# Performance work log

Measured on AMD Instinct MI355X. Metric: run time of the kernel, lower is better.

## Reference

```python
import jax, jax.numpy as jnp
import numpy as np

T = 4096          # total tokens across ragged segments
H = 4096          # hidden_size
I = 11008         # intermediate_size
R = 16            # lora_rank
A = 4             # number of adapters (segments)


def setup_inputs() -> dict:
    key = jax.random.key(0)
    ks = jax.random.split(key, 12)
    inp = {
        "x": jax.random.normal(ks[0], (T, H), jnp.float32),
        "gate_w": jax.random.normal(ks[1], (I, H), jnp.float32) * (1.0 / np.sqrt(H)),
        "up_w": jax.random.normal(ks[2], (I, H), jnp.float32) * (1.0 / np.sqrt(H)),
        "down_w": jax.random.normal(ks[3], (H, I), jnp.float32) * (1.0 / np.sqrt(I)),
        "gate_wa": jax.random.normal(ks[4], (A, H, R), jnp.float32) * 0.01,
        "gate_wb": jax.random.normal(ks[5], (A, R, I), jnp.float32) * 0.01,
        "up_wa": jax.random.normal(ks[6], (A, H, R), jnp.float32) * 0.01,
        "up_wb": jax.random.normal(ks[7], (A, R, I), jnp.float32) * 0.01,
        "down_wa": jax.random.normal(ks[8], (A, I, R), jnp.float32) * 0.01,
        "down_wb": jax.random.normal(ks[9], (A, R, H), jnp.float32) * 0.01,
        "seg_ids": jnp.sort(jax.random.randint(ks[10], (T,), 0, A, jnp.int32)),
    }
    return inp


def _add_lora(y, inp, wa, wb, mask):
    # Segment-batched low-rank GEMM (Punica/S-LoRA add_lora):
    # for token t in segment a:  y[t] += inp[t] @ wa[a] @ wb[a]
    # mask: [T, A] one-hot of token->adapter assignment.
    # [A, T, R]: project into rank space for every adapter (R tiny), mask out
    xa = jnp.einsum('th,ahr->tar', inp, wa) * mask[:, :, None]   # [T, A, R]
    a, r = wb.shape[0], wb.shape[1]
    # collapse (A, R) so the expansion is one GEMM, no [A, T, out] intermediate
    delta = xa.reshape(inp.shape[0], a * r) @ wb.reshape(a * r, wb.shape[2])
    return y + delta


def reference(x, gate_w, up_w, down_w, gate_wa, gate_wb, up_wa, up_wb,
              down_wa, down_wb, seg_ids):
    mask = (seg_ids[:, None] == jnp.arange(A, dtype=seg_ids.dtype)[None, :]
            ).astype(x.dtype)                                    # [T, A]
    gate = x @ gate_w.T                                          # [T, I]
    gate = _add_lora(gate, x, gate_wa, gate_wb, mask)
    gate = jax.nn.silu(gate)
    up = x @ up_w.T                                              # [T, I]
    up = _add_lora(up, x, up_wa, up_wb, mask)
    t = gate * up
    down = t @ down_w.T                                          # [T, H]
    down = _add_lora(down, t, down_wa, down_wb, mask)
    return down
```

## Files before the change

kernel.cpp:

```cpp
#include <hip/hip_runtime.h>

#define T_TOK 4096
#define HID   4096
#define IMD   11008

using f32x4  = __attribute__((ext_vector_type(4))) float;
using bf16x8 = __attribute__((ext_vector_type(8))) __bf16;
union FragCast { int4 i; bf16x8 b; };

__device__ __forceinline__ unsigned f2bf_bits(float f) {
  unsigned u = __float_as_uint(f);
  return (u + 0x7fffu + ((u >> 16) & 1u)) >> 16;
}
__device__ __forceinline__ float bf2f(short s) {
  return __uint_as_float(((unsigned)(unsigned short)s) << 16);
}
__device__ __forceinline__ int4 cvt8(const float4 f0, const float4 f1) {
  int4 r;
  r.x = f2bf_bits(f0.x) | (f2bf_bits(f0.y) << 16);
  r.y = f2bf_bits(f0.z) | (f2bf_bits(f0.w) << 16);
  r.z = f2bf_bits(f1.x) | (f2bf_bits(f1.y) << 16);
  r.w = f2bf_bits(f1.z) | (f2bf_bits(f1.w) << 16);
  return r;
}
__device__ __forceinline__ void gload16(const void* g, void* l) {
  __builtin_amdgcn_global_load_lds(
      (__attribute__((address_space(1))) void*)g,
      (__attribute__((address_space(3))) void*)l, 16, 0, 0);
}

__global__ void cvt_pad(const float* __restrict__ in, short* __restrict__ out,
                        int C8, int CT, long ldin, long ldout) {
  long r = blockIdx.x;
  const float4* s = (const float4*)(in + r * ldin);
  int4* d = (int4*)(out + r * ldout);
  for (int c = threadIdx.x; c < CT; c += blockDim.x)
    d[c] = (c < C8) ? cvt8(s[2 * c], s[2 * c + 1]) : int4{0, 0, 0, 0};
}

__global__ void build_wbT_pad(const float* __restrict__ wb,
                              short* __restrict__ out, int N, long ldout,
                              long K) {
  int n = blockIdx.x * blockDim.x + threadIdx.x;
  int ar = blockIdx.y;
  if (n < N) out[(long)n * ldout + K + ar] = (short)f2bf_bits(wb[(long)ar * N + n]);
}

template <int KD, int NOUT>
__global__ __launch_bounds__(256)
void lora_proj(const short* __restrict__ Abf, long ldA,
               const float* __restrict__ wa0, const float* __restrict__ wa1,
               const int* __restrict__ seg, short* out0, long ld0, short* out1,
               long ld1) {
  __shared__ __align__(16) short rowbuf[KD];
  __shared__ float part[NOUT][4][16];
  int t = blockIdx.x, tid = threadIdx.x;
  int a = seg[t];
  const int4* src = (const int4*)(Abf + (long)t * ldA);
  for (int c = tid; c < KD / 8; c += 256) ((int4*)rowbuf)[c] = src[c];
  __syncthreads();
  int w = tid >> 6, l = tid & 63;
  int r = l & 15, g = l >> 4;
  const int HW = KD / 4;
  float s0 = 0.f, s1 = 0.f;
  const float* p0 = wa0 + (long)a * KD * 16 + r;
  const float* p1 = (NOUT == 2) ? (wa1 + (long)a * KD * 16 + r) : nullptr;
  int h = w * HW + g;
  for (int k = 0; k < HW / 4; ++k, h += 4) {
    float xv = bf2f(rowbuf[h]);
    s0 = fmaf(xv, p0[(long)h * 16], s0);
    if (NOUT == 2) s1 = fmaf(xv, p1[(long)h * 16], s1);
  }
  s0 += __shfl_xor(s0, 16); s0 += __shfl_xor(s0, 32);
  if (NOUT == 2) { s1 += __shfl_xor(s1, 16); s1 += __shfl_xor(s1, 32); }
  if (l < 16) { part[0][w][r] = s0; if (NOUT == 2) part[1][w][r] = s1; }
  __syncthreads();
  if (tid < 64 * NOUT) {
    int m = tid >> 6, ar = tid & 63;
    float v = 0.f;
    if ((ar >> 4) == a) {
      int r2 = ar & 15;
      v = part[m][0][r2] + part[m][1][r2] + part[m][2][r2] + part[m][3][r2];
    }
    short b = (short)f2bf_bits(v);
    if (m == 0) out0[(long)t * ld0 + ar] = b;
    else        out1[(long)t * ld1 + ar] = b;
  }
}

template <int MODE>
__global__ __launch_bounds__(512, 2)
void gemm_gu(const short* __restrict__ A, const short* __restrict__ B,
             const short* __restrict__ gbuf, short* __restrict__ outB,
             int tilesPerXcd, long ldK, int iters, long ldo) {
  extern __shared__ __align__(16) char smem[];

  int xcd = blockIdx.x & 7, loc = blockIdx.x >> 3;
  int tid = threadIdx.x;
  int l = tid & 63, wid = tid >> 6;
  int wr = wid >> 2, wc = wid & 3;
  int lrow = l & 15, lhi = l >> 4, md = lrow & 7;
  const int rr0 = tid >> 3;
  const long cOff = (long)(((tid & 7) ^ (rr0 & 7)) * 8);

  const int csel0 = (lhi ^ md) * 16;
  const int csel1 = ((4 + lhi) ^ md) * 16;

  const short* pA; const short* pB; long row0, col0;
  auto setTile = [&](int idxInXcd) {
    int gt = xcd * tilesPerXcd + idxInXcd;
    row0 = (long)(gt & 15) * 256;
    col0 = (long)(gt >> 4) * 256;
    pA = A + (row0 + rr0) * ldK + cOff;
    pB = B + (col0 + rr0) * ldK + cOff;
  };
  auto stA = [&](int bi, int h, int kt) {
    char* d = smem + bi * 32768 + tid * 16;
    const short* s = pA + (long)kt * 64 + (long)(2 * h) * 64 * ldK;
    gload16(s, d + (2 * h) * 8192);
    gload16(s + (long)64 * ldK, d + (2 * h + 1) * 8192);
  };
  auto stB = [&](int bi, int h, int kt) {
    char* d = smem + 98304 + bi * 32768 + tid * 16;
    const short* s = pB + (long)kt * 64 + (long)(2 * h) * 64 * ldK;
    gload16(s, d + (2 * h) * 8192);
    gload16(s + (long)64 * ldK, d + (2 * h + 1) * 8192);
  };
  auto prologue = [&]() {
    stA(0, 0, 0); stA(0, 1, 0);
    stB(0, 0, 0); stB(0, 1, 0);
    stA(1, 0, 1); stA(1, 1, 1);
  };

  f32x4 zr = {0.f, 0.f, 0.f, 0.f};

  int r = loc;
  setTile(r);
  prologue();

  while (true) {
    f32x4 acc[8][4];
#pragma unroll
    for (int mi = 0; mi < 8; ++mi)
#pragma unroll
      for (int ni = 0; ni < 4; ++ni) acc[mi][ni] = zr;

    asm volatile("s_waitcnt vmcnt(4)" ::: "memory");
    asm volatile("s_barrier" ::: "memory");

    int ca = 0;
#pragma unroll 1
    for (int t = 0; t < iters; ++t) {
      const char* Ab = smem + ca * 32768;
      const char* Bb = smem + 98304 + (t & 1) * 32768;
      int na2 = (ca >= 1) ? ca - 1 : 2;
      int nb1 = (t + 1) & 1;
      bf16x8 bF[4][2];

#pragma unroll
      for (int p = 0; p < 4; ++p) {
        if (p == 0) {
#pragma unroll
          for (int ni = 0; ni < 4; ++ni) {
            const char* base = Bb + (wc * 64 + ni * 16 + lrow) * 128;
            FragCast f0, f1;
            f0.i = *(const int4*)(base + csel0);
            f1.i = *(const int4*)(base + csel1);
            bF[ni][0] = f0.b; bF[ni][1] = f1.b;
          }
        }
        bf16x8 aF[2][2];
#pragma unroll
        for (int m2 = 0; m2 < 2; ++m2) {
          const char* base = Ab + (wr * 128 + p * 32 + m2 * 16 + lrow) * 128;
          FragCast f0, f1;
          f0.i = *(const int4*)(base + csel0);
          f1.i = *(const int4*)(base + csel1);
          aF[m2][0] = f0.b; aF[m2][1] = f1.b;
        }
        if (p == 0 && t + 1 < iters) stB(nb1, 0, t + 1);
        if (p == 1 && t + 1 < iters) stB(nb1, 1, t + 1);
        if (p == 2 && t + 2 < iters) stA(na2, 0, t + 2);
        if (p == 3) {
          if (t + 2 < iters) {
            stA(na2, 1, t + 2);
            asm volatile("s_waitcnt vmcnt(4)" ::: "memory");
          } else {
            asm volatile("s_waitcnt vmcnt(0)" ::: "memory");
          }
        }
        asm volatile("s_barrier" ::: "memory");
        __builtin_amdgcn_s_setprio(1);
#pragma unroll
        for (int k = 0; k < 2; ++k)
#pragma unroll
          for (int m2 = 0; m2 < 2; ++m2)
#pragma unroll
            for (int ni = 0; ni < 4; ++ni)
              acc[p * 2 + m2][ni] = __builtin_amdgcn_mfma_f32_16x16x32_bf16(
                  aF[m2][k], bF[ni][k], acc[p * 2 + m2][ni], 0, 0, 0);
        __builtin_amdgcn_s_setprio(0);
        asm volatile("s_barrier" ::: "memory");
      }
      ca = (ca == 2) ? 0 : ca + 1;
    }

    long crow = row0, ccol = col0;
    r += 32;
    bool hasNext = (r < tilesPerXcd);
    if (hasNext) { setTile(r); prologue(); }

#pragma unroll
    for (int mi = 0; mi < 8; ++mi)
#pragma unroll
      for (int ni = 0; ni < 4; ++ni)
#pragma unroll
        for (int j = 0; j < 4; ++j) {
          long grow = crow + wr * 128 + mi * 16 + lhi * 4 + j;
          long gcol = ccol + wc * 64 + ni * 16 + lrow;
          long idx = grow * ldo + gcol;
          float v = acc[mi][ni][j];
          if constexpr (MODE == 0) {
            outB[idx] = (short)f2bf_bits(v);
          } else {
            float g = bf2f(gbuf[idx]);
            float t2 = g * (1.f / (1.f + __expf(-g))) * v;
            outB[idx] = (short)f2bf_bits(t2);
          }
        }
    if (!hasNext) break;
  }
}

__global__ __launch_bounds__(512, 2)
void gemm_down(const short* __restrict__ A, const short* __restrict__ B,
               float* outF, int nby, long ldK, int iters, long ldo) {
  extern __shared__ __align__(16) char smem[];

  int nwg = gridDim.x;
  int orig = blockIdx.x;
  int q = nwg >> 3, rr = nwg & 7;
  int xcd = orig & 7, loc = orig >> 3;
  int swz = (xcd < rr ? xcd * (q + 1) : rr * (q + 1) + (xcd - rr) * q) + loc;
  int by = swz % nby, bx = swz / nby;
  long row0 = (long)bx * 256, col0 = (long)by * 256;

  int tid = threadIdx.x;
  int l = tid & 63, wid = tid >> 6;
  int wr = wid >> 2, wc = wid & 3;
  int lrow = l & 15, lhi = l >> 4, md = lrow & 7;

  const short* aP[4]; const short* bP[4];
  int dst[4];
#pragma unroll
  for (int k = 0; k < 4; ++k) {
    int idx = tid + k * 512;
    int r = idx >> 3, c8 = idx & 7;
    aP[k] = A + (row0 + r) * ldK + (c8 ^ (r & 7)) * 8;
    bP[k] = B + (col0 + r) * ldK + (c8 ^ (r & 7)) * 8;
    dst[k] = idx * 16;
  }

  auto stageA_h = [&](int bi, int h) {
    char* d = smem + bi * 32768;
    gload16(aP[2 * h], d + dst[2 * h]);         aP[2 * h] += 64;
    gload16(aP[2 * h + 1], d + dst[2 * h + 1]); aP[2 * h + 1] += 64;
  };
  auto stageB_h = [&](int bi, int h) {
    char* d = smem + 98304 + bi * 32768;
    gload16(bP[2 * h], d + dst[2 * h]);         bP[2 * h] += 64;
    gload16(bP[2 * h + 1], d + dst[2 * h + 1]); bP[2 * h + 1] += 64;
  };

  f32x4 acc[8][4];
  f32x4 zr = {0.f, 0.f, 0.f, 0.f};
#pragma unroll
  for (int mi = 0; mi < 8; ++mi)
#pragma unroll
    for (int ni = 0; ni < 4; ++ni) acc[mi][ni] = zr;

  const int csel0 = (lhi ^ md) * 16;
  const int csel1 = ((4 + lhi) ^ md) * 16;

  stageA_h(0, 0); stageA_h(0, 1);
  stageB_h(0, 0); stageB_h(0, 1);
  stageA_h(1, 0); stageA_h(1, 1);
  asm volatile("s_waitcnt vmcnt(4)" ::: "memory");
  asm volatile("s_barrier" ::: "memory");

  int ca = 0;
#pragma unroll 1
  for (int t = 0; t < iters; ++t) {
    const char* Ab = smem + ca * 32768;
    const char* Bb = smem + 98304 + (t & 1) * 32768;
    int na2 = (ca >= 1) ? ca - 1 : 2;
    int nb1 = (t + 1) & 1;
    bf16x8 bF[4][2];

#pragma unroll
    for (int p = 0; p < 4; ++p) {
      if (p == 0) {
#pragma unroll
        for (int ni = 0; ni < 4; ++ni) {
          const char* base = Bb + (wc * 64 + ni * 16 + lrow) * 128;
          FragCast f0, f1;
          f0.i = *(const int4*)(base + csel0);
          f1.i = *(const int4*)(base + csel1);
          bF[ni][0] = f0.b; bF[ni][1] = f1.b;
        }
      }
      bf16x8 aF[2][2];
#pragma unroll
      for (int m2 = 0; m2 < 2; ++m2) {
        const char* base = Ab + (wr * 128 + p * 32 + m2 * 16 + lrow) * 128;
        FragCast f0, f1;
        f0.i = *(const int4*)(base + csel0);
        f1.i = *(const int4*)(base + csel1);
        aF[m2][0] = f0.b; aF[m2][1] = f1.b;
      }
      if (p == 0 && t + 1 < iters) stageB_h(nb1, 0);
      if (p == 1 && t + 1 < iters) stageB_h(nb1, 1);
      if (p == 2 && t + 2 < iters) stageA_h(na2, 0);
      if (p == 3) {
        if (t + 2 < iters) {
          stageA_h(na2, 1);
          asm volatile("s_waitcnt vmcnt(4)" ::: "memory");
        } else {
          asm volatile("s_waitcnt vmcnt(0)" ::: "memory");
        }
      }
      asm volatile("s_barrier" ::: "memory");
      __builtin_amdgcn_s_setprio(1);
#pragma unroll
      for (int k = 0; k < 2; ++k)
#pragma unroll
        for (int m2 = 0; m2 < 2; ++m2)
#pragma unroll
          for (int ni = 0; ni < 4; ++ni)
            acc[p * 2 + m2][ni] = __builtin_amdgcn_mfma_f32_16x16x32_bf16(
                aF[m2][k], bF[ni][k], acc[p * 2 + m2][ni], 0, 0, 0);
      __builtin_amdgcn_s_setprio(0);
      asm volatile("s_barrier" ::: "memory");
    }
    ca = (ca == 2) ? 0 : ca + 1;
  }

#pragma unroll
  for (int mi = 0; mi < 8; ++mi)
#pragma unroll
    for (int ni = 0; ni < 4; ++ni)
#pragma unroll
      for (int j = 0; j < 4; ++j) {
        long grow = row0 + wr * 128 + mi * 16 + lhi * 4 + j;
        long gcol = col0 + wc * 64 + ni * 16 + lrow;
        outF[grow * ldo + gcol] = acc[mi][ni][j];
      }
}

extern "C" void kernel_launch(void* const* d_in, const int* in_sizes, int n_in,
                              void* d_out, int out_size, void* d_ws,
                              size_t ws_size, hipStream_t stream) {
  const float* x       = (const float*)d_in[0];
  const float* gate_w  = (const float*)d_in[1];
  const float* up_w    = (const float*)d_in[2];
  const float* down_w  = (const float*)d_in[3];
  const float* gate_wa = (const float*)d_in[4];
  const float* gate_wb = (const float*)d_in[5];
  const float* up_wa   = (const float*)d_in[6];
  const float* up_wb   = (const float*)d_in[7];
  const float* down_wa = (const float*)d_in[8];
  const float* down_wb = (const float*)d_in[9];
  const int*   seg     = (const int*)d_in[10];

  char* ws = (char*)d_ws;
  short* xg_pad = (short*)(ws);
  short* wA     = (short*)(ws + 34603008);
  short* wB     = (short*)(ws + 127598592);
  short* t_pad  = (short*)(ws + 220594176);

  const int LDS_G = 163840;
  hipFuncSetAttribute(reinterpret_cast<const void*>(&gemm_gu<0>),
                      hipFuncAttributeMaxDynamicSharedMemorySize, LDS_G);
  hipFuncSetAttribute(reinterpret_cast<const void*>(&gemm_gu<1>),
                      hipFuncAttributeMaxDynamicSharedMemorySize, LDS_G);
  hipFuncSetAttribute(reinterpret_cast<const void*>(&gemm_down),
                      hipFuncAttributeMaxDynamicSharedMemorySize, LDS_G);

  cvt_pad<<<T_TOK, 256, 0, stream>>>(x, xg_pad, 512, 512, HID, 4224);
  cvt_pad<<<IMD, 256, 0, stream>>>(gate_w, wA, 512, 528, HID, 4224);
  cvt_pad<<<IMD, 256, 0, stream>>>(up_w, wB, 512, 528, HID, 4224);
  build_wbT_pad<<<dim3(43, 64), 256, 0, stream>>>(gate_wb, wA, IMD, 4224, 4096);
  build_wbT_pad<<<dim3(43, 64), 256, 0, stream>>>(up_wb, wB, IMD, 4224, 4160);
  lora_proj<HID, 2><<<T_TOK, 256, 0, stream>>>(
      xg_pad, 4224, gate_wa, up_wa, seg, xg_pad + 4096, 4224, xg_pad + 4160,
      4224);

  gemm_gu<0><<<256, 512, LDS_G, stream>>>(xg_pad, wA, nullptr, t_pad,
                                          86, 4224, 66, 11072);
  gemm_gu<1><<<256, 512, LDS_G, stream>>>(xg_pad, wB, t_pad, t_pad,
                                          86, 4224, 66, 11072);

  cvt_pad<<<T_TOK, 256, 0, stream>>>(down_w, wA, 1376, 1376, IMD, 11072);
  build_wbT_pad<<<dim3(16, 64), 256, 0, stream>>>(down_wb, wA, HID, 11072,
                                                  IMD);
  lora_proj<IMD, 1><<<T_TOK, 256, 0, stream>>>(
      t_pad, 11072, down_wa, nullptr, seg, t_pad + IMD, 11072, nullptr, 64);

  gemm_down<<<16 * 16, 512, LDS_G, stream>>>(t_pad, wA, (float*)d_out, 16,
                                             11072, 173, 4096);
}
```

Before: 1.650 ms.

## Fuse gate and up GEMMs into one kernel, restructure K-loop into two half-phases

Replaces the two separate gate and up GEMM launches with one kernel that, per output tile, computes the gate GEMM and then the up GEMM with the SiLU-multiply epilogue. The epilogue reads back the gate values it just wrote, so they are likely still in cache. The inner K-loop in both the fused kernel and gemm_down drops the four-phase schedule with a barrier per phase for two half-tile phases with fewer barriers, and larger A fragment loads. This cuts one launch and the barrier count, but removes the overlap of the next tile's prologue with the epilogue and raises register pressure from holding more fragments.

```diff
diff --git a/kernel.cpp b/kernel.cpp
--- a/kernel.cpp
+++ b/kernel.cpp
@@ -88,11 +88,10 @@
   }
 }
 
-template <int MODE>
 __global__ __launch_bounds__(512, 2)
-void gemm_gu(const short* __restrict__ A, const short* __restrict__ B,
-             const short* __restrict__ gbuf, short* __restrict__ outB,
-             int tilesPerXcd, long ldK, int iters, long ldo) {
+void gemm_guc(const short* __restrict__ A, const short* __restrict__ Bg,
+              const short* __restrict__ Bu, short* __restrict__ tpad,
+              int tilesPerXcd, long ldK, int iters, long ldo) {
   extern __shared__ __align__(16) char smem[];
 
   int xcd = blockIdx.x & 7, loc = blockIdx.x >> 3;
@@ -106,14 +105,9 @@
   const int csel0 = (lhi ^ md) * 16;
   const int csel1 = ((4 + lhi) ^ md) * 16;
 
-  const short* pA; const short* pB; long row0, col0;
-  auto setTile = [&](int idxInXcd) {
-    int gt = xcd * tilesPerXcd + idxInXcd;
-    row0 = (long)(gt & 15) * 256;
-    col0 = (long)(gt >> 4) * 256;
-    pA = A + (row0 + rr0) * ldK + cOff;
-    pB = B + (col0 + rr0) * ldK + cOff;
-  };
+  long row0, col0;
+  const short* pA; const short* pB;
+
   auto stA = [&](int bi, int h, int kt) {
     char* d = smem + bi * 32768 + tid * 16;
     const short* s = pA + (long)kt * 64 + (long)(2 * h) * 64 * ldK;
@@ -126,115 +120,124 @@
     gload16(s, d + (2 * h) * 8192);
     gload16(s + (long)64 * ldK, d + (2 * h + 1) * 8192);
   };
-  auto prologue = [&]() {
-    stA(0, 0, 0); stA(0, 1, 0);
-    stB(0, 0, 0); stB(0, 1, 0);
-    stA(1, 0, 1); stA(1, 1, 1);
-  };
 
   f32x4 zr = {0.f, 0.f, 0.f, 0.f};
 
-  int r = loc;
-  setTile(r);
-  prologue();
-
-  while (true) {
-    f32x4 acc[8][4];
-#pragma unroll
-    for (int mi = 0; mi < 8; ++mi)
-#pragma unroll
-      for (int ni = 0; ni < 4; ++ni) acc[mi][ni] = zr;
-
-    asm volatile("s_waitcnt vmcnt(4)" ::: "memory");
-    asm volatile("s_barrier" ::: "memory");
-
-    int ca = 0;
+  for (int r = loc; r < tilesPerXcd; r += 32) {
+    int gt = xcd * tilesPerXcd + r;
+    row0 = (long)(gt & 15) * 256;
+    col0 = (long)(gt >> 4) * 256;
+    pA = A + (row0 + rr0) * ldK + cOff;
+
+    for (int pass = 0; pass < 2; ++pass) {
+      pB = (pass ? Bu : Bg) + (col0 + rr0) * ldK + cOff;
+
+      stA(0, 0, 0); stA(0, 1, 0);
+      stB(0, 0, 0); stB(0, 1, 0);
+      stA(1, 0, 1); stA(1, 1, 1);
+      asm volatile("s_waitcnt vmcnt(4)" ::: "memory");
+      asm volatile("s_barrier" ::: "memory");
+
+      f32x4 acc[8][4];
+#pragma unroll
+      for (int mi = 0; mi < 8; ++mi)
+#pragma unroll
+        for (int ni = 0; ni < 4; ++ni) acc[mi][ni] = zr;
+
+      int ca = 0;
 #pragma unroll 1
-    for (int t = 0; t < iters; ++t) {
-      const char* Ab = smem + ca * 32768;
-      const char* Bb = smem + 98304 + (t & 1) * 32768;
-      int na2 = (ca >= 1) ? ca - 1 : 2;
-      int nb1 = (t + 1) & 1;
-      bf16x8 bF[4][2];
-
-#pragma unroll
-      for (int p = 0; p < 4; ++p) {
-        if (p == 0) {
-#pragma unroll
-          for (int ni = 0; ni < 4; ++ni) {
-            const char* base = Bb + (wc * 64 + ni * 16 + lrow) * 128;
-            FragCast f0, f1;
-            f0.i = *(const int4*)(base + csel0);
-            f1.i = *(const int4*)(base + csel1);
-            bF[ni][0] = f0.b; bF[ni][1] = f1.b;
-          }
-        }
-        bf16x8 aF[2][2];
-#pragma unroll
-        for (int m2 = 0; m2 < 2; ++m2) {
-          const char* base = Ab + (wr * 128 + p * 32 + m2 * 16 + lrow) * 128;
+      for (int t = 0; t < iters; ++t) {
+        const char* Ab = smem + ca * 32768;
+        const char* Bb = smem + 98304 + (t & 1) * 32768;
+        int na2 = (ca >= 1) ? ca - 1 : 2;
+        int nb1 = (t + 1) & 1;
+
+        bf16x8 bF[4][2], aL[4][2];
+#pragma unroll
+        for (int ni = 0; ni < 4; ++ni) {
+          const char* base = Bb + (wc * 64 + ni * 16 + lrow) * 128;
           FragCast f0, f1;
           f0.i = *(const int4*)(base + csel0);
           f1.i = *(const int4*)(base + csel1);
-          aF[m2][0] = f0.b; aF[m2][1] = f1.b;
+          bF[ni][0] = f0.b; bF[ni][1] = f1.b;
         }
-        if (p == 0 && t + 1 < iters) stB(nb1, 0, t + 1);
-        if (p == 1 && t + 1 < iters) stB(nb1, 1, t + 1);
-        if (p == 2 && t + 2 < iters) stA(na2, 0, t + 2);
-        if (p == 3) {
-          if (t + 2 < iters) {
-            stA(na2, 1, t + 2);
-            asm volatile("s_waitcnt vmcnt(4)" ::: "memory");
-          } else {
-            asm volatile("s_waitcnt vmcnt(0)" ::: "memory");
-          }
+#pragma unroll
+        for (int m2 = 0; m2 < 4; ++m2) {
+          const char* base = Ab + (wr * 128 + m2 * 16 + lrow) * 128;
+          FragCast f0, f1;
+          f0.i = *(const int4*)(base + csel0);
+          f1.i = *(const int4*)(base + csel1);
+          aL[m2][0] = f0.b; aL[m2][1] = f1.b;
         }
+        if (t + 1 < iters) { stB(nb1, 0, t + 1); stB(nb1, 1, t + 1); }
         asm volatile("s_barrier" ::: "memory");
         __builtin_amdgcn_s_setprio(1);
 #pragma unroll
         for (int k = 0; k < 2; ++k)
 #pragma unroll
-          for (int m2 = 0; m2 < 2; ++m2)
+          for (int m2 = 0; m2 < 4; ++m2)
 #pragma unroll
             for (int ni = 0; ni < 4; ++ni)
-              acc[p * 2 + m2][ni] = __builtin_amdgcn_mfma_f32_16x16x32_bf16(
-                  aF[m2][k], bF[ni][k], acc[p * 2 + m2][ni], 0, 0, 0);
+              acc[m2][ni] = __builtin_amdgcn_mfma_f32_16x16x32_bf16(
+                  aL[m2][k], bF[ni][k], acc[m2][ni], 0, 0, 0);
         __builtin_amdgcn_s_setprio(0);
-        asm volatile("s_barrier" ::: "memory");
+
+        bf16x8 aH[4][2];
+#pragma unroll
+        for (int m2 = 0; m2 < 4; ++m2) {
+          const char* base = Ab + (wr * 128 + 64 + m2 * 16 + lrow) * 128;
+          FragCast f0, f1;
+          f0.i = *(const int4*)(base + csel0);
+          f1.i = *(const int4*)(base + csel1);
+          aH[m2][0] = f0.b; aH[m2][1] = f1.b;
+        }
+        if (t + 2 < iters) {
+          stA(na2, 0, t + 2); stA(na2, 1, t + 2);
+          asm volatile("s_waitcnt vmcnt(4)" ::: "memory");
+          asm volatile("s_barrier" ::: "memory");
+        } else if (t + 1 < iters) {
+          asm volatile("s_waitcnt vmcnt(0)" ::: "memory");
+          asm volatile("s_barrier" ::: "memory");
+        }
+        __builtin_amdgcn_s_setprio(1);
+#pragma unroll
+        for (int k = 0; k < 2; ++k)
+#pragma unroll
+          for (int m2 = 0; m2 < 4; ++m2)
+#pragma unroll
+            for (int ni = 0; ni < 4; ++ni)
+              acc[4 + m2][ni] = __builtin_amdgcn_mfma_f32_16x16x32_bf16(
+                  aH[m2][k], bF[ni][k], acc[4 + m2][ni], 0, 0, 0);
+        __builtin_amdgcn_s_setprio(0);
+        ca = (ca == 2) ? 0 : ca + 1;
       }
-      ca = (ca == 2) ? 0 : ca + 1;
-    }
-
-    long crow = row0, ccol = col0;
-    r += 32;
-    bool hasNext = (r < tilesPerXcd);
-    if (hasNext) { setTile(r); prologue(); }
-
-#pragma unroll
-    for (int mi = 0; mi < 8; ++mi)
-#pragma unroll
-      for (int ni = 0; ni < 4; ++ni)
-#pragma unroll
-        for (int j = 0; j < 4; ++j) {
-          long grow = crow + wr * 128 + mi * 16 + lhi * 4 + j;
-          long gcol = ccol + wc * 64 + ni * 16 + lrow;
-          long idx = grow * ldo + gcol;
-          float v = acc[mi][ni][j];
-          if constexpr (MODE == 0) {
-            outB[idx] = (short)f2bf_bits(v);
-          } else {
-            float g = bf2f(gbuf[idx]);
-            float t2 = g * (1.f / (1.f + __expf(-g))) * v;
-            outB[idx] = (short)f2bf_bits(t2);
+
+#pragma unroll
+      for (int mi = 0; mi < 8; ++mi)
+#pragma unroll
+        for (int ni = 0; ni < 4; ++ni)
+#pragma unroll
+          for (int j = 0; j < 4; ++j) {
+            long grow = row0 + wr * 128 + mi * 16 + lhi * 4 + j;
+            long gcol = col0 + wc * 64 + ni * 16 + lrow;
+            long idx = grow * ldo + gcol;
+            float v = acc[mi][ni][j];
+            if (pass == 0) {
+              tpad[idx] = (short)f2bf_bits(v);
+            } else {
+              float g = bf2f(tpad[idx]);
+              float t2 = g * (1.f / (1.f + __expf(-g))) * v;
+              tpad[idx] = (short)f2bf_bits(t2);
+            }
           }
-        }
-    if (!hasNext) break;
+    }
   }
 }
 
 __global__ __launch_bounds__(512, 2)
 void gemm_down(const short* __restrict__ A, const short* __restrict__ B,
-               float* outF, int nby, long ldK, int iters, long ldo) {
+               float* __restrict__ outF, int nby, long ldK, int iters,
+               long ldo) {
   extern __shared__ __align__(16) char smem[];
 
   int nwg = gridDim.x;
@@ -249,27 +252,26 @@
   int l = tid & 63, wid = tid >> 6;
   int wr = wid >> 2, wc = wid & 3;
   int lrow = l & 15, lhi = l >> 4, md = lrow & 7;
-
-  const short* aP[4]; const short* bP[4];
-  int dst[4];
-#pragma unroll
-  for (int k = 0; k < 4; ++k) {
-    int idx = tid + k * 512;
-    int r = idx >> 3, c8 = idx & 7;
-    aP[k] = A + (row0 + r) * ldK + (c8 ^ (r & 7)) * 8;
-    bP[k] = B + (col0 + r) * ldK + (c8 ^ (r & 7)) * 8;
-    dst[k] = idx * 16;
-  }
-
-  auto stageA_h = [&](int bi, int h) {
-    char* d = smem + bi * 32768;
-    gload16(aP[2 * h], d + dst[2 * h]);         aP[2 * h] += 64;
-    gload16(aP[2 * h + 1], d + dst[2 * h + 1]); aP[2 * h + 1] += 64;
+  const int rr0 = tid >> 3;
+  const long cOff = (long)(((tid & 7) ^ (rr0 & 7)) * 8);
+
+  const int csel0 = (lhi ^ md) * 16;
+  const int csel1 = ((4 + lhi) ^ md) * 16;
+
+  const short* pA = A + (row0 + rr0) * ldK + cOff;
+  const short* pB = B + (col0 + rr0) * ldK + cOff;
+
+  auto stA = [&](int bi, int h, int kt) {
+    char* d = smem + bi * 32768 + tid * 16;
+    const short* s = pA + (long)kt * 64 + (long)(2 * h) * 64 * ldK;
+    gload16(s, d + (2 * h) * 8192);
+    gload16(s + (long)64 * ldK, d + (2 * h + 1) * 8192);
   };
-  auto stageB_h = [&](int bi, int h) {
-    char* d = smem + 98304 + bi * 32768;
-    gload16(bP[2 * h], d + dst[2 * h]);         bP[2 * h] += 64;
-    gload16(bP[2 * h + 1], d + dst[2 * h + 1]); bP[2 * h + 1] += 64;
+  auto stB = [&](int bi, int h, int kt) {
+    char* d = smem + 98304 + bi * 32768 + tid * 16;
+    const short* s = pB + (long)kt * 64 + (long)(2 * h) * 64 * ldK;
+    gload16(s, d + (2 * h) * 8192);
+    gload16(s + (long)64 * ldK, d + (2 * h + 1) * 8192);
   };
 
   f32x4 acc[8][4];
@@ -279,12 +281,9 @@
 #pragma unroll
     for (int ni = 0; ni < 4; ++ni) acc[mi][ni] = zr;
 
-  const int csel0 = (lhi ^ md) * 16;
-  const int csel1 = ((4 + lhi) ^ md) * 16;
-
-  stageA_h(0, 0); stageA_h(0, 1);
-  stageB_h(0, 0); stageB_h(0, 1);
-  stageA_h(1, 0); stageA_h(1, 1);
+  stA(0, 0, 0); stA(0, 1, 0);
+  stB(0, 0, 0); stB(0, 1, 0);
+  stA(1, 0, 1); stA(1, 1, 1);
   asm volatile("s_waitcnt vmcnt(4)" ::: "memory");
   asm volatile("s_barrier" ::: "memory");
 
@@ -295,53 +294,64 @@
     const char* Bb = smem + 98304 + (t & 1) * 32768;
     int na2 = (ca >= 1) ? ca - 1 : 2;
     int nb1 = (t + 1) & 1;
-    bf16x8 bF[4][2];
-
-#pragma unroll
-    for (int p = 0; p < 4; ++p) {
-      if (p == 0) {
-#pragma unroll
-        for (int ni = 0; ni < 4; ++ni) {
-          const char* base = Bb + (wc * 64 + ni * 16 + lrow) * 128;
-          FragCast f0, f1;
-          f0.i = *(const int4*)(base + csel0);
-          f1.i = *(const int4*)(base + csel1);
-          bF[ni][0] = f0.b; bF[ni][1] = f1.b;
-        }
-      }
-      bf16x8 aF[2][2];
-#pragma unroll
-      for (int m2 = 0; m2 < 2; ++m2) {
-        const char* base = Ab + (wr * 128 + p * 32 + m2 * 16 + lrow) * 128;
-        FragCast f0, f1;
-        f0.i = *(const int4*)(base + csel0);
-        f1.i = *(const int4*)(base + csel1);
-        aF[m2][0] = f0.b; aF[m2][1] = f1.b;
-      }
-      if (p == 0 && t + 1 < iters) stageB_h(nb1, 0);
-      if (p == 1 && t + 1 < iters) stageB_h(nb1, 1);
-      if (p == 2 && t + 2 < iters) stageA_h(na2, 0);
-      if (p == 3) {
-        if (t + 2 < iters) {
-          stageA_h(na2, 1);
-          asm volatile("s_waitcnt vmcnt(4)" ::: "memory");
-        } else {
-          asm volatile("s_waitcnt vmcnt(0)" ::: "memory");
-        }
-      }
+
+    bf16x8 bF[4][2], aL[4][2];
+#pragma unroll
+    for (int ni = 0; ni < 4; ++ni) {
+      const char* base = Bb + (wc * 64 + ni * 16 + lrow) * 128;
+      FragCast f0, f1;
+      f0.i = *(const int4*)(base + csel0);
+      f1.i = *(const int4*)(base + csel1);
+      bF[ni][0] = f0.b; bF[ni][1] = f1.b;
+    }
+#pragma unroll
+    for (int m2 = 0; m2 < 4; ++m2) {
+      const char* base = Ab + (wr * 128 + m2 * 16 + lrow) * 128;
+      FragCast f0, f1;
+      f0.i = *(const int4*)(base + csel0);
+      f1.i = *(const int4*)(base + csel1);
+      aL[m2][0] = f0.b; aL[m2][1] = f1.b;
+    }
+    if (t + 1 < iters) { stB(nb1, 0, t + 1); stB(nb1, 1, t + 1); }
+    asm volatile("s_barrier" ::: "memory");
+    __builtin_amdgcn_s_setprio(1);
+#pragma unroll
+    for (int k = 0; k < 2; ++k)
+#pragma unroll
+      for (int m2 = 0; m2 < 4; ++m2)
+#pragma unroll
+        for (int ni = 0; ni < 4; ++ni)
+          acc[m2][ni] = __builtin_amdgcn_mfma_f32_16x16x32_bf16(
+              aL[m2][k], bF[ni][k], acc[m2][ni], 0, 0, 0);
+    __builtin_amdgcn_s_setprio(0);
+
+    bf16x8 aH[4][2];
+#pragma unroll
+    for (int m2 = 0; m2 < 4; ++m2) {
+      const char* base = Ab + (wr * 128 + 64 + m2 * 16 + lrow) * 128;
+      FragCast f0, f1;
+      f0.i = *(const int4*)(base + csel0);
+      f1.i = *(const int4*)(base + csel1);
+      aH[m2][0] = f0.b; aH[m2][1] = f1.b;
+    }
+    if (t + 2 < iters) {
+      stA(na2, 0, t + 2); stA(na2, 1, t + 2);
+      asm volatile("s_waitcnt vmcnt(4)" ::: "memory");
       asm volatile("s_barrier" ::: "memory");
-      __builtin_amdgcn_s_setprio(1);
-#pragma unroll
-      for (int k = 0; k < 2; ++k)
-#pragma unroll
-        for (int m2 = 0; m2 < 2; ++m2)
-#pragma unroll
-          for (int ni = 0; ni < 4; ++ni)
-            acc[p * 2 + m2][ni] = __builtin_amdgcn_mfma_f32_16x16x32_bf16(
-                aF[m2][k], bF[ni][k], acc[p * 2 + m2][ni], 0, 0, 0);
-      __builtin_amdgcn_s_setprio(0);
+    } else if (t + 1 < iters) {
+      asm volatile("s_waitcnt vmcnt(0)" ::: "memory");
       asm volatile("s_barrier" ::: "memory");
     }
+    __builtin_amdgcn_s_setprio(1);
+#pragma unroll
+    for (int k = 0; k < 2; ++k)
+#pragma unroll
+      for (int m2 = 0; m2 < 4; ++m2)
+#pragma unroll
+        for (int ni = 0; ni < 4; ++ni)
+          acc[4 + m2][ni] = __builtin_amdgcn_mfma_f32_16x16x32_bf16(
+              aH[m2][k], bF[ni][k], acc[4 + m2][ni], 0, 0, 0);
+    __builtin_amdgcn_s_setprio(0);
     ca = (ca == 2) ? 0 : ca + 1;
   }
 
@@ -379,9 +389,7 @@
   short* t_pad  = (short*)(ws + 220594176);
 
   const int LDS_G = 163840;
-  hipFuncSetAttribute(reinterpret_cast<const void*>(&gemm_gu<0>),
-                      hipFuncAttributeMaxDynamicSharedMemorySize, LDS_G);
-  hipFuncSetAttribute(reinterpret_cast<const void*>(&gemm_gu<1>),
+  hipFuncSetAttribute(reinterpret_cast<const void*>(&gemm_guc),
                       hipFuncAttributeMaxDynamicSharedMemorySize, LDS_G);
   hipFuncSetAttribute(reinterpret_cast<const void*>(&gemm_down),
                       hipFuncAttributeMaxDynamicSharedMemorySize, LDS_G);
@@ -395,10 +403,8 @@
       xg_pad, 4224, gate_wa, up_wa, seg, xg_pad + 4096, 4224, xg_pad + 4160,
       4224);
 
-  gemm_gu<0><<<256, 512, LDS_G, stream>>>(xg_pad, wA, nullptr, t_pad,
-                                          86, 4224, 66, 11072);
-  gemm_gu<1><<<256, 512, LDS_G, stream>>>(xg_pad, wB, t_pad, t_pad,
-                                          86, 4224, 66, 11072);
+  gemm_guc<<<256, 512, LDS_G, stream>>>(xg_pad, wA, wB, t_pad,
+                                        86, 4224, 66, 11072);
 
   cvt_pad<<<T_TOK, 256, 0, stream>>>(down_w, wA, 1376, 1376, IMD, 11072);
   build_wbT_pad<<<dim3(16, 64), 256, 0, stream>>>(down_wb, wA, HID, 11072,
```

Measured after the change: 1.547 ms. -6.3%, faster.
